# Kernel tuning notes

Measured on AMD Instinct MI355X. Metric: run time of the kernel, lower is better.

The kernel has to match this reference:

```python
import jax, jax.numpy as jnp
import numpy as np

GAMMA = 0.25
GN_EPS = 1e-5


def setup_inputs() -> dict:
    key = jax.random.key(0)
    k1, k2, k3 = jax.random.split(key, 3)
    B, T, C = 16, 2048, 512
    G, V, Dv = 2, 320, 256
    x = jax.random.normal(k1, (B, T, C), dtype=jnp.float32)
    conv_w = jax.random.normal(k2, (G, C // G, C // G), dtype=jnp.float32) * 0.05
    gn_w = jnp.ones((C,), dtype=jnp.float32)
    gn_b = jnp.zeros((C,), dtype=jnp.float32)
    emb = 0.01 * jax.random.normal(k3, (V, G, Dv), dtype=jnp.float32)
    return {"x": x, "conv_w": conv_w, "gn_w": gn_w, "gn_b": gn_b, "emb": emb}


def _vq_forward(x, conv_w, gn_w, gn_b, emb):
    B, T, C = x.shape
    V, G, Dv = emb.shape
    sg = jax.lax.stop_gradient
    # time_first -> BxCxT
    xt = jnp.transpose(x, (0, 2, 1))  # [B,C,T]
    # grouped 1x1 conv (no bias)
    xg = xt.reshape(B, G, C // G, T)
    ze = jnp.einsum('goi,bgit->bgot', conv_w, xg)  # [B,G,C/G,T]
    # Fp32GroupNorm over (C/G, T) per group, biased variance
    zf = ze.astype(jnp.float32)
    mu = jnp.mean(zf, axis=(2, 3), keepdims=True)
    var = jnp.mean(jnp.square(zf - mu), axis=(2, 3), keepdims=True)
    zn = ((zf - mu) * jax.lax.rsqrt(var + GN_EPS)).reshape(B, C, T)
    ze = (zn * gn_w[None, :, None] + gn_b[None, :, None]).astype(ze.dtype)  # [B,C,T]
    # split into groups along feature dim: [B,T,G,Dv]
    ze_ = jnp.transpose(ze.reshape(B, G, Dv, T), (0, 3, 1, 2))
    # squared distances [V,B,T,G] (argmin of ||.||_2 == argmin of ||.||_2^2)
    d2 = (jnp.sum(jnp.square(ze_), axis=-1)[None]
          - 2.0 * jnp.einsum('btgd,vgd->vbtg', ze_, emb)
          + jnp.sum(jnp.square(emb), axis=-1)[:, None, None, :])
    idx = jnp.argmin(d2, axis=0)  # [B,T,G] int
    # gather nearest codewords per group
    zq = emb[idx, jnp.arange(G)[None, None, :]]  # [B,T,G,Dv]
    zq = jnp.transpose(zq.reshape(B, T, C), (0, 2, 1))  # [B,C,T]
    # straight-through
    out = sg(zq) + (ze - sg(ze))  # [B,C,T]
    # code perplexity (no grad)
    probs = jnp.mean(jax.nn.one_hot(sg(idx), V, dtype=jnp.float32), axis=(0, 1))  # [G,V]
    perplexity = jnp.sum(jnp.exp(-jnp.sum(probs * jnp.log(probs + 1e-7), axis=-1)))
    # losses
    zef, zqf = ze.astype(jnp.float32), zq.astype(jnp.float32)
    latent = jnp.mean(jnp.square(zqf - sg(zef)))
    commit = jnp.mean(jnp.square(zef - sg(zqf)))
    loss = latent + GAMMA * commit
    out = jnp.transpose(out, (0, 2, 1))  # back to BxTxC
    return out, loss, perplexity, idx


def reference(x, conv_w, gn_w, gn_b, emb):
    return _vq_forward(x, conv_w, gn_w, gn_b, emb)
```

## Files before the change

kernel.cpp:

```cpp
#include <hip/hip_runtime.h>

#define Bq 16
#define Tq 2048
#define Cq 512
#define Gq 2
#define CGq 256
#define Vq 320
#define Mq 32768
#define LOSS_OFF 16777216
#define PPL_OFF  16777217
#define IDX_OFF  16777218

#define MARGIN 1.75e-4f
#define LIST_CAP 16384
#define LIST2_CAP 1024

#define WS_PCONV 0
#define WS_PLOSS 16384
#define WS_MU    49152
#define WS_RS    49280
#define WS_E2    49408
#define WS_LOSSF 51968
#define WS_CNT   51976
#define WS_CNT2  51980
#define WS_HIST  51984
#define WS_PL2   54544
#define WS_LIST2 70928
#define WS_WSP   131072
#define WS_LISTQ 917504

#define SL(X, r) ((X) * 16 + ((r) ^ ((X) & 7)))

typedef short s16x8 __attribute__((ext_vector_type(8)));
typedef float f32x4v __attribute__((ext_vector_type(4)));

__device__ __forceinline__ void bsplit(float x, unsigned &b1, unsigned &b2) {
    unsigned u = __float_as_uint(x);
    unsigned r1 = (u + 0x7fffu + ((u >> 16) & 1u)) & 0xffff0000u;
    b1 = r1 >> 16;
    float d = x - __uint_as_float(r1);
    unsigned u2 = __float_as_uint(d);
    b2 = (u2 + 0x7fffu + ((u2 >> 16) & 1u)) >> 16;
}

__device__ __forceinline__ void bsplit3(float x, unsigned &h, unsigned &m, unsigned &l) {
    unsigned u = __float_as_uint(x);
    unsigned r1 = (u + 0x7fffu + ((u >> 16) & 1u)) & 0xffff0000u;
    h = r1 >> 16;
    float d1 = x - __uint_as_float(r1);
    unsigned u2 = __float_as_uint(d1);
    unsigned r2 = (u2 + 0x7fffu + ((u2 >> 16) & 1u)) & 0xffff0000u;
    m = r2 >> 16;
    float d2 = d1 - __uint_as_float(r2);
    unsigned u3 = __float_as_uint(d2);
    l = (u3 + 0x7fffu + ((u3 >> 16) & 1u)) >> 16;
}

__global__ __launch_bounds__(256) void k_e2(const float* __restrict__ emb,
                                            float* __restrict__ e2w) {
    int row  = blockIdx.x * 4 + (threadIdx.x >> 6);
    int lane = threadIdx.x & 63;
    float4 v = *(const float4*)(emb + (size_t)row * 256 + lane * 4);
    float s = v.x * v.x + v.y * v.y + v.z * v.z + v.w * v.w;
#pragma unroll
    for (int m = 1; m < 64; m <<= 1) s += __shfl_xor(s, m);
    if (lane == 0) e2w[(row & 1) * Vq + (row >> 1)] = s;
}

__global__ __launch_bounds__(256) void k_wsplit(const float* __restrict__ w,
                                                unsigned char* __restrict__ wsp) {
    int t = blockIdx.x * 256 + threadIdx.x;
    int g = t >> 13, o = (t >> 5) & 255, ihi = t & 31;
    const float* src = w + ((size_t)(g * 256 + o)) * 256 + ihi * 8;
    float xv[8];
    *(float4*)(xv + 0) = *(const float4*)(src);
    *(float4*)(xv + 4) = *(const float4*)(src + 4);
    unsigned ph[4] = {0,0,0,0}, pm[4] = {0,0,0,0}, pl[4] = {0,0,0,0};
#pragma unroll
    for (int e = 0; e < 8; e++) {
        unsigned h, m, l;
        bsplit3(xv[e], h, m, l);
        ph[e >> 1] |= h << ((e & 1) * 16);
        pm[e >> 1] |= m << ((e & 1) * 16);
        pl[e >> 1] |= l << ((e & 1) * 16);
    }
    int kc = ihi >> 2, quad = ihi & 3, ct = o >> 4, lf = o & 15;
    size_t base = (size_t)(g * 3) * 131072 + (size_t)kc * 16384 + ct * 1024 + quad * 256 + lf * 16;
    *(uint4*)(wsp + base + 0 * 131072) = *(uint4*)ph;
    *(uint4*)(wsp + base + 1 * 131072) = *(uint4*)pm;
    *(uint4*)(wsp + base + 2 * 131072) = *(uint4*)pl;
}

__global__ __launch_bounds__(256) void k_esplit(const float* __restrict__ emb,
                                                unsigned char* __restrict__ esp) {
    int t = blockIdx.x * 256 + threadIdx.x;
    int g  = t / 10240;
    int r  = t - g * 10240;
    int kc = r / 1280;
    int r2 = r - kc * 1280;
    int ct = r2 >> 6;
    int r3 = r2 & 63;
    int kq = r3 >> 4, l15 = r3 & 15;
    int v  = ct * 16 + l15;
    int k0 = kc * 32 + kq * 8;
    const float* src = emb + ((size_t)v * 2 + g) * 256 + k0;
    float xv[8];
    *(float4*)(xv + 0) = *(const float4*)(src);
    *(float4*)(xv + 4) = *(const float4*)(src + 4);
    unsigned ph[4] = {0,0,0,0}, pl[4] = {0,0,0,0};
#pragma unroll
    for (int e = 0; e < 8; e++) {
        unsigned h, l;
        bsplit(xv[e], h, l);
        ph[e >> 1] |= h << ((e & 1) * 16);
        pl[e >> 1] |= l << ((e & 1) * 16);
    }
    size_t base = (size_t)g * 327680 + (size_t)kc * 20480
                + (size_t)((ct * 4 + kq) * 16 + l15) * 16;
    *(uint4*)(esp + base) = *(uint4*)ph;
    *(uint4*)(esp + base + 163840) = *(uint4*)pl;
}

__global__ __launch_bounds__(256, 2) void k_convM(const float* __restrict__ x,
    const unsigned char* __restrict__ wsp, float* __restrict__ ze,
    double* __restrict__ pconv)
{
    __shared__ unsigned char lds[73728];
    __shared__ double reds[4], redq[4];
    uint4* Bs = (uint4*)lds;
    uint4* As = (uint4*)(lds + 49152);

    int tid = threadIdx.x, bx = blockIdx.x;
    int mt = bx >> 1, g = bx & 1;
    int m0 = mt * 128;
    int w = tid >> 6, lane = tid & 63;
    int quad = lane >> 4, l15 = lane & 15;
    int arow = tid >> 1, ah = tid & 1;
    int aw = arow >> 5, art = (arow >> 4) & 1, ar = arow & 15;
    const float* xrow = x + (size_t)(m0 + arow) * Cq + g * CGq + ah * 16;
    const unsigned char* wslab = wsp + (size_t)(g * 3) * 131072;

    f32x4v zero4 = {0.f, 0.f, 0.f, 0.f};
    f32x4v acc[2][16];
#pragma unroll
    for (int i = 0; i < 2; i++)
#pragma unroll
        for (int j = 0; j < 16; j++) acc[i][j] = zero4;

    for (int kc = 0; kc < 8; kc++) {
        if (kc) __syncthreads();
#pragma unroll
        for (int j = 0; j < 12; j++) {
            int L = (w * 12 + j) * 1024 + lane * 16;
            int p = L >> 14, r = L & 16383;
            __builtin_amdgcn_global_load_lds(
                (const __attribute__((address_space(1))) void*)(wslab + (size_t)p * 131072 + (size_t)kc * 16384 + r),
                (__attribute__((address_space(3))) void*)(lds + L), 16, 0, 0);
        }
// ... 34 lines not shown
#pragma unroll
            for (int rt = 0; rt < 2; rt++) {
                acc[rt][ct] = __builtin_amdgcn_mfma_f32_16x16x32_bf16(afr[0][rt], b0, acc[rt][ct], 0, 0, 0);
                acc[rt][ct] = __builtin_amdgcn_mfma_f32_16x16x32_bf16(afr[1][rt], b0, acc[rt][ct], 0, 0, 0);
                acc[rt][ct] = __builtin_amdgcn_mfma_f32_16x16x32_bf16(afr[2][rt], b0, acc[rt][ct], 0, 0, 0);
                acc[rt][ct] = __builtin_amdgcn_mfma_f32_16x16x32_bf16(afr[0][rt], b1, acc[rt][ct], 0, 0, 0);
                acc[rt][ct] = __builtin_amdgcn_mfma_f32_16x16x32_bf16(afr[1][rt], b1, acc[rt][ct], 0, 0, 0);
                acc[rt][ct] = __builtin_amdgcn_mfma_f32_16x16x32_bf16(afr[0][rt], b2, acc[rt][ct], 0, 0, 0);
            }
        }
    }

    float s = 0.f, q = 0.f;
    float* zb = ze + (size_t)m0 * Cq + g * CGq;
#pragma unroll
    for (int rt = 0; rt < 2; rt++)
#pragma unroll
    for (int ct = 0; ct < 16; ct++)
#pragma unroll
    for (int j = 0; j < 4; j++) {
        float v = acc[rt][ct][j];
        zb[(size_t)(w * 32 + rt * 16 + quad * 4 + j) * Cq + ct * 16 + l15] = v;
        s += v;
        q = __builtin_fmaf(v, v, q);
    }
    double ds = (double)s, dq = (double)q;
#pragma unroll
    for (int m = 1; m < 64; m <<= 1) { ds += __shfl_xor(ds, m); dq += __shfl_xor(dq, m); }
    if (lane == 0) { reds[w] = ds; redq[w] = dq; }
    __syncthreads();
    if (tid == 0) {
        pconv[bx * 2 + 0] = reds[0] + reds[1] + reds[2] + reds[3];
        pconv[bx * 2 + 1] = redq[0] + redq[1] + redq[2] + redq[3];
    }
}

__global__ __launch_bounds__(256) void k_stats(const double* __restrict__ pconv,
                                               float* __restrict__ muw,
                                               float* __restrict__ rsw) {
    int tid = threadIdx.x;
    int bg = tid >> 3, r = tid & 7;
    int b = bg >> 1, g = bg & 1;
    double s = 0.0, q = 0.0;
    for (int j = r; j < 16; j += 8) {
        int pi = (b * 16 + j) * 2 + g;
        s += pconv[pi * 2 + 0];
        q += pconv[pi * 2 + 1];
    }
#pragma unroll
    for (int m = 1; m < 8; m <<= 1) { s += __shfl_xor(s, m); q += __shfl_xor(q, m); }
    if (r == 0) {
        double mu = s / 524288.0;
        double var = q / 524288.0 - mu * mu;
        double rs = 1.0 / sqrt(var + 1e-5);
        muw[bg] = (float)mu;
        rsw[bg] = (float)rs;
    }
}

__global__ __launch_bounds__(256, 2) void k_distA(const unsigned char* __restrict__ esp,
    const float* __restrict__ gw, const float* __restrict__ gb,
    const float* __restrict__ muw, const float* __restrict__ rsw,
    const float* __restrict__ e2w, float* dout,
    unsigned* __restrict__ cntw, unsigned* __restrict__ cnt2w,
    unsigned long long* __restrict__ listq, unsigned* __restrict__ list2)
{
    __shared__ uint4 Asl[1024];
    __shared__ unsigned char ldsB[40960];
    __shared__ float e2s[Vq];
    uint4* Bsl = (uint4*)ldsB;

    int tid = threadIdx.x, bx = blockIdx.x;
    int mt = bx >> 1, g = bx & 1;
    int m0 = mt * 128;
    int bg = (m0 >> 11) * 2 + g;
    float muf = muw[bg], rsf = rsw[bg];
    int w = tid >> 6, lane = tid & 63;
    int quad = lane >> 4, l15 = lane & 15;

    for (int i = tid; i < Vq; i += 256) e2s[i] = e2w[g * Vq + i];

    int arow = tid >> 1, ah = tid & 1;
    int aw = arow >> 5, art = (arow >> 4) & 1, ar = arow & 15;
    const float* zrow = dout + (size_t)m0 * Cq + g * CGq + (size_t)arow * Cq;
    const unsigned char* eslab = esp + (size_t)g * 327680;

    f32x4v zero4 = {0.f, 0.f, 0.f, 0.f};
    f32x4v acc[2][20];
#pragma unroll
    for (int i = 0; i < 2; i++)
#pragma unroll
        for (int j = 0; j < 20; j++) acc[i][j] = zero4;

    for (int kc8 = 0; kc8 < 8; kc8++) {
        if (kc8) __syncthreads();
        int k0 = kc8 * 32;
#pragma unroll
        for (int j = 0; j < 10; j++) {
            int L = j * 4096 + tid * 16;
            int s = (j >= 5) ? 1 : 0;
            __builtin_amdgcn_global_load_lds(
                (const __attribute__((address_space(1))) void*)(eslab + (size_t)s * 143360 + (size_t)kc8 * 20480 + L),
// ... 37 lines not shown
        for (int ct = 0; ct < 20; ct++) {
            s16x8 b0 = __builtin_bit_cast(s16x8, Bsl[((0*20 + ct)*4 + quad)*16 + l15]);
            s16x8 b1 = __builtin_bit_cast(s16x8, Bsl[((1*20 + ct)*4 + quad)*16 + l15]);
#pragma unroll
            for (int rt = 0; rt < 2; rt++) {
                acc[rt][ct] = __builtin_amdgcn_mfma_f32_16x16x32_bf16(afr[0][rt], b0, acc[rt][ct], 0, 0, 0);
                acc[rt][ct] = __builtin_amdgcn_mfma_f32_16x16x32_bf16(afr[0][rt], b1, acc[rt][ct], 0, 0, 0);
                acc[rt][ct] = __builtin_amdgcn_mfma_f32_16x16x32_bf16(afr[1][rt], b0, acc[rt][ct], 0, 0, 0);
            }
        }
    }

#pragma unroll
    for (int rt = 0; rt < 2; rt++)
#pragma unroll
    for (int j = 0; j < 4; j++) {
        float m1 = 3.402823466e+38f; int i1 = 0;
#pragma unroll
        for (int ct = 0; ct < 20; ct++) {
            float d2a = e2s[ct * 16 + l15] - 2.0f * acc[rt][ct][j];
            if (d2a < m1) { m1 = d2a; i1 = ct * 16 + l15; }
        }
#pragma unroll
        for (int mm = 1; mm < 16; mm <<= 1) {
            float ov = __shfl_xor(m1, mm);
            int   oi = __shfl_xor(i1, mm);
            if (ov < m1 || (ov == m1 && oi < i1)) { m1 = ov; i1 = oi; }
        }
        float thr = m1 + MARGIN;
        unsigned mask = 0;
#pragma unroll
        for (int ct = 0; ct < 20; ct++) {
            float d2a = e2s[ct * 16 + l15] - 2.0f * acc[rt][ct][j];
            if (d2a <= thr) mask |= (1u << ct);
        }
        int cnt = __popc(mask);
#pragma unroll
        for (int mm = 1; mm < 16; mm <<= 1) cnt += __shfl_xor(cnt, mm);
        int mrow = m0 + w * 32 + rt * 16 + quad * 4 + j;
        unsigned q = (unsigned)mrow * 2u + (unsigned)g;
        unsigned flag = 0;
        if (cnt > 1) {
            if ((i1 & 15) == l15) mask &= ~(1u << (i1 >> 4));
            int cl2 = __popc(mask);
            int inc = cl2;
#pragma unroll
            for (int off = 1; off < 16; off <<= 1) {
                int t = __shfl_up(inc, off, 16);
                if (l15 >= off) inc += t;
            }
            int pre = inc - cl2;
            if (cnt <= 5) {
                int pos_ = 0;
                if (l15 == 0) pos_ = (int)atomicAdd(cntw, 1u);
                pos_ = __shfl(pos_, 0, 16);
                if ((unsigned)pos_ < LIST_CAP) {
                    flag = 512u;
                    unsigned long long contrib = 0ull;
                    unsigned mm2 = mask; int k = pre;
                    while (mm2) {
                        int ct2 = __ffs(mm2) - 1; mm2 &= mm2 - 1;
                        contrib |= ((unsigned long long)(unsigned)(ct2 * 16 + l15)) << (20 + 9 * k);
                        k++;
                    }
#pragma unroll
                    for (int mm = 1; mm < 16; mm <<= 1)
                        contrib |= __shfl_xor(contrib, mm);
                    if (l15 == 0)
                        listq[pos_] = (unsigned long long)q
                                    | ((unsigned long long)(unsigned)cnt << 17) | contrib;
                }
            } else {
                if (l15 == 0) {
                    unsigned p2 = atomicAdd(cnt2w, 1u);
                    if (p2 < LIST2_CAP) { list2[p2] = q; flag = 512u; }
                }
            }
        }
        if (l15 == 0) dout[IDX_OFF + q] = __uint_as_float((unsigned)i1 | flag);
    }
}

__global__ __launch_bounds__(256) void k_exS(const float* __restrict__ emb,
    const float* __restrict__ gw, const float* __restrict__ gb,
    const float* __restrict__ muw, const float* __restrict__ rsw,
    const float* __restrict__ e2w, float* dout,
    unsigned* __restrict__ hist, double* __restrict__ ploss)
{
    int tid = threadIdx.x;
    int lane = tid & 63;
    int wid = blockIdx.x * 4 + (tid >> 6);
    int quad = lane >> 2, j = lane & 3;
    int q = wid * 16 + quad;
    int m = q >> 1, g = q & 1;
    int bg = (m >> 11) * 2 + g;
    float muf = muw[bg], rsf = rsw[bg];
    unsigned packed = __float_as_uint(dout[IDX_OFF + q]);
    int flag = (packed >> 9) & 1;
    int v = packed & 511;
    const float* zb  = dout + (size_t)m * Cq + g * CGq;
    const float* gwb = gw + g * CGq;
    const float* gbb = gb + g * CGq;
    const float* eb  = emb + ((size_t)v * Gq + g) * CGq;
    float z2p = 0.f, dp = 0.f;
    for (int kc = 0; kc < 16; kc++) {
        int k0 = kc * 16 + j * 4;
        float4 z  = *(const float4*)(zb + k0);
        float4 gv = *(const float4*)(gwb + k0);
        float4 bv = *(const float4*)(gbb + k0);
        float4 e4 = *(const float4*)(eb + k0);
        float zn0 = __fadd_rn(__fmul_rn(__fmul_rn(__fsub_rn(z.x, muf), rsf), gv.x), bv.x);
        float zn1 = __fadd_rn(__fmul_rn(__fmul_rn(__fsub_rn(z.y, muf), rsf), gv.y), bv.y);
        float zn2 = __fadd_rn(__fmul_rn(__fmul_rn(__fsub_rn(z.z, muf), rsf), gv.z), bv.z);
        float zn3 = __fadd_rn(__fmul_rn(__fmul_rn(__fsub_rn(z.w, muf), rsf), gv.w), bv.w);
        z2p = __builtin_fmaf(zn0, zn0, z2p);
        z2p = __builtin_fmaf(zn1, zn1, z2p);
        z2p = __builtin_fmaf(zn2, zn2, z2p);
        z2p = __builtin_fmaf(zn3, zn3, z2p);
        dp = __builtin_fmaf(zn0, e4.x, dp);
        dp = __builtin_fmaf(zn1, e4.y, dp);
        dp = __builtin_fmaf(zn2, e4.z, dp);
        dp = __builtin_fmaf(zn3, e4.w, dp);
    }
    z2p += __shfl_xor(z2p, 1); z2p += __shfl_xor(z2p, 2);
    dp  += __shfl_xor(dp, 1);  dp  += __shfl_xor(dp, 2);
    float d2 = __fadd_rn(__fsub_rn(z2p, 2.0f * dp), e2w[g * Vq + v]);
    double lp = 0.0;
    if (!flag && j == 0) {
        dout[IDX_OFF + q] = (float)v;
        atomicAdd(&hist[g * Vq + v], 1u);
        lp = (double)d2;
    }
#pragma unroll
    for (int mm = 1; mm < 64; mm <<= 1) lp += __shfl_xor(lp, mm);
    if (lane == 0) ploss[wid] = lp;
}

__global__ __launch_bounds__(256) void k_exF3(const float* __restrict__ emb,
    const float* __restrict__ gw, const float* __restrict__ gb,
    const float* __restrict__ muw, const float* __restrict__ rsw,
    const float* __restrict__ e2w, float* dout,
    unsigned* __restrict__ hist, double* __restrict__ ploss2,
    const unsigned long long* __restrict__ listq, const unsigned* __restrict__ cntw)
{
    int tid = threadIdx.x, lane = tid & 63;
    int gwid = blockIdx.x * 4 + (tid >> 6);
    int cslot = lane >> 2, j = lane & 3;
    unsigned nn = *cntw; if (nn > LIST_CAP) nn = LIST_CAP;
    int n = (int)nn;
    double lacc = 0.0;
    for (int it = gwid; it < n; it += 2048) {
        unsigned long long e = listq[it];
        unsigned q = (unsigned)(e & 0x1FFFFull);
        int cnt = (int)((e >> 17) & 7u);
        int m = (int)(q >> 1), g = (int)(q & 1u);
        int bg = (m >> 11) * 2 + g;
        float muf = muw[bg], rsf = rsw[bg];
        int v = (int)(__float_as_uint(dout[IDX_OFF + q]) & 511u);
        if (cslot >= 1 && cslot < cnt)
            v = (int)((e >> (20 + 9 * (cslot - 1))) & 511ull);
        const float* zb  = dout + (size_t)m * Cq + g * CGq;
        const float* gwb = gw + g * CGq;
        const float* gbb = gb + g * CGq;
        const float* eb  = emb + ((size_t)v * Gq + g) * CGq;
        float z2p = 0.f, dp = 0.f;
        for (int kc = 0; kc < 16; kc++) {
            int k0 = kc * 16 + j * 4;
            float4 z  = *(const float4*)(zb + k0);
            float4 gv = *(const float4*)(gwb + k0);
            float4 bv = *(const float4*)(gbb + k0);
            float4 e4 = *(const float4*)(eb + k0);
            float zn0 = __fadd_rn(__fmul_rn(__fmul_rn(__fsub_rn(z.x, muf), rsf), gv.x), bv.x);
            float zn1 = __fadd_rn(__fmul_rn(__fmul_rn(__fsub_rn(z.y, muf), rsf), gv.y), bv.y);
            float zn2 = __fadd_rn(__fmul_rn(__fmul_rn(__fsub_rn(z.z, muf), rsf), gv.z), bv.z);
            float zn3 = __fadd_rn(__fmul_rn(__fmul_rn(__fsub_rn(z.w, muf), rsf), gv.w), bv.w);
            z2p = __builtin_fmaf(zn0, zn0, z2p);
            z2p = __builtin_fmaf(zn1, zn1, z2p);
            z2p = __builtin_fmaf(zn2, zn2, z2p);
            z2p = __builtin_fmaf(zn3, zn3, z2p);
            dp = __builtin_fmaf(zn0, e4.x, dp);
            dp = __builtin_fmaf(zn1, e4.y, dp);
            dp = __builtin_fmaf(zn2, e4.z, dp);
            dp = __builtin_fmaf(zn3, e4.w, dp);
        }
        z2p += __shfl_xor(z2p, 1); z2p += __shfl_xor(z2p, 2);
        dp  += __shfl_xor(dp, 1);  dp  += __shfl_xor(dp, 2);
        float d2 = __fadd_rn(__fsub_rn(z2p, 2.0f * dp), e2w[g * Vq + v]);
#pragma unroll
        for (int mm = 4; mm < 64; mm <<= 1) {
            float od = __shfl_xor(d2, mm);
            int   ov = __shfl_xor(v, mm);
            if (od < d2 || (od == d2 && ov < v)) { d2 = od; v = ov; }
        }
        if (lane == 0) {
            dout[IDX_OFF + q] = (float)v;
            atomicAdd(&hist[g * Vq + v], 1u);
            lacc += (double)d2;
        }
    }
    if (lane == 0) ploss2[gwid] = lacc;
}

__global__ __launch_bounds__(256) void k_exFslow(const float* __restrict__ emb,
    const float* __restrict__ gw, const float* __restrict__ gb,
    const float* __restrict__ muw, const float* __restrict__ rsw,
    const float* __restrict__ e2w, float* dout,
    unsigned* __restrict__ hist, double* __restrict__ lossf,
    const unsigned* __restrict__ cnt2w, const unsigned* __restrict__ list2)
{
    int tid = threadIdx.x, lane = tid & 63;
    int wid = blockIdx.x * 4 + (tid >> 6);
    unsigned nn = *cnt2w; if (nn > LIST2_CAP) nn = LIST2_CAP;
    int n = (int)nn;
    for (int it = wid; it < n; it += 128) {
        int q = (int)list2[it];
        int m = q >> 1, g = q & 1;
        int bg = (m >> 11) * 2 + g;
        float muf = muw[bg], rsf = rsw[bg];
        const float* zb = dout + (size_t)m * Cq + g * CGq;
        int k0 = lane * 4;
        float4 z  = *(const float4*)(zb + k0);
        float4 gv = *(const float4*)(gw + g * CGq + k0);
        float4 bv = *(const float4*)(gb + g * CGq + k0);
        float zn0 = __fadd_rn(__fmul_rn(__fmul_rn(__fsub_rn(z.x, muf), rsf), gv.x), bv.x);
        float zn1 = __fadd_rn(__fmul_rn(__fmul_rn(__fsub_rn(z.y, muf), rsf), gv.y), bv.y);
        float zn2 = __fadd_rn(__fmul_rn(__fmul_rn(__fsub_rn(z.z, muf), rsf), gv.z), bv.z);
        float zn3 = __fadd_rn(__fmul_rn(__fmul_rn(__fsub_rn(z.w, muf), rsf), gv.w), bv.w);
        float s = 0.f;
        for (int kc = 0; kc < 16; kc++) {
            int src = (lane & 3) + kc * 4;
            float a0 = __shfl(zn0, src), a1 = __shfl(zn1, src);
            float a2 = __shfl(zn2, src), a3 = __shfl(zn3, src);
            s = __builtin_fmaf(a0, a0, s);
            s = __builtin_fmaf(a1, a1, s);
            s = __builtin_fmaf(a2, a2, s);
            s = __builtin_fmaf(a3, a3, s);
        }
        s += __shfl_xor(s, 1); s += __shfl_xor(s, 2);
        float z2 = s;
        float m1 = 3.402823466e+38f; int i1 = 0;
        for (int v = 0; v < Vq; v += 2) {
            const float* e0 = emb + ((size_t)v * Gq + g) * CGq + k0;
            float4 ea = *(const float4*)e0;
            float4 eb4 = *(const float4*)(e0 + Gq * CGq);
            float da = zn0 * ea.x;  da = __builtin_fmaf(zn1, ea.y, da);
            da = __builtin_fmaf(zn2, ea.z, da); da = __builtin_fmaf(zn3, ea.w, da);
            float db = zn0 * eb4.x; db = __builtin_fmaf(zn1, eb4.y, db);
// ... 2 lines not shown
            for (int mm = 1; mm < 64; mm <<= 1) { da += __shfl_xor(da, mm); db += __shfl_xor(db, mm); }
            float d2a = __fadd_rn(__fsub_rn(z2, 2.0f * da), e2w[g * Vq + v]);
            float d2b = __fadd_rn(__fsub_rn(z2, 2.0f * db), e2w[g * Vq + v + 1]);
            if (d2a < m1) { m1 = d2a; i1 = v; }
            if (d2b < m1) { m1 = d2b; i1 = v + 1; }
        }
        if (lane == 0) {
            dout[IDX_OFF + q] = (float)i1;
            atomicAdd(&hist[g * Vq + i1], 1u);
            atomicAdd(lossf, (double)m1);
        }
    }
}

__global__ __launch_bounds__(256) void k_out(const float* __restrict__ emb, float* dout) {
    size_t u = (size_t)blockIdx.x * 256 + threadIdx.x;
    size_t pos = u * 4;
    int m = (int)(pos >> 9);
    int c = (int)(pos & 511);
    int g = c >> 8, d = c & 255;
    int v = (int)dout[IDX_OFF + (size_t)m * Gq + g];
    float4 o = *(const float4*)(emb + ((size_t)(v * 2 + g)) * 256 + d);
    *(float4*)(dout + pos) = o;
}

__global__ __launch_bounds__(256) void k_final(const double* __restrict__ ploss,
                                               const double* __restrict__ ploss2,
                                               const double* __restrict__ lossf,
                                               const unsigned* __restrict__ hist,
                                               float* dout) {
    __shared__ double redl[4], red0[4], red1[4];
    int tid = threadIdx.x;
    double s = 0.0;
    for (int i = tid; i < 4096; i += 256) s += ploss[i];
    for (int i = tid; i < 2048; i += 256) s += ploss2[i];
#pragma unroll
    for (int m = 1; m < 64; m <<= 1) s += __shfl_xor(s, m);
    double e0 = 0.0, e1 = 0.0;
    for (int pid = tid; pid < 640; pid += 256) {
        double p = (double)hist[pid] * (1.0 / 32768.0);
        double t = p * log(p + 1e-7);
        if (pid < 320) e0 += t; else e1 += t;
    }
#pragma unroll
    for (int m = 1; m < 64; m <<= 1) { e0 += __shfl_xor(e0, m); e1 += __shfl_xor(e1, m); }
    int lane = tid & 63, wv_ = tid >> 6;
    if (lane == 0) { redl[wv_] = s; red0[wv_] = e0; red1[wv_] = e1; }
    __syncthreads();
    if (tid == 0) {
        double S  = redl[0] + redl[1] + redl[2] + redl[3] + *lossf;
        double E0 = red0[0] + red0[1] + red0[2] + red0[3];
        double E1 = red1[0] + red1[1] + red1[2] + red1[3];
        dout[LOSS_OFF] = (float)(1.25 * S / 16777216.0);
        dout[PPL_OFF]  = (float)(exp(-E0) + exp(-E1));
    }
}

extern "C" void kernel_launch(void* const* d_in, const int* in_sizes, int n_in,
                              void* d_out, int out_size, void* d_ws, size_t ws_size,
                              hipStream_t stream) {
    const float* x   = (const float*)d_in[0];
    const float* w   = (const float*)d_in[1];
    const float* gw  = (const float*)d_in[2];
    const float* gb  = (const float*)d_in[3];
    const float* emb = (const float*)d_in[4];
    float* dout = (float*)d_out;
    char* ws = (char*)d_ws;
    double* pconv   = (double*)(ws + WS_PCONV);
    double* ploss   = (double*)(ws + WS_PLOSS);
    float* muw      = (float*)(ws + WS_MU);
    float* rsw      = (float*)(ws + WS_RS);
    float* e2w      = (float*)(ws + WS_E2);
    double* lossf   = (double*)(ws + WS_LOSSF);
    unsigned* cntw  = (unsigned*)(ws + WS_CNT);
    unsigned* cnt2w = (unsigned*)(ws + WS_CNT2);
    unsigned* hist  = (unsigned*)(ws + WS_HIST);
    double* ploss2  = (double*)(ws + WS_PL2);
    unsigned* list2 = (unsigned*)(ws + WS_LIST2);
    unsigned char* wsp = (unsigned char*)(ws + WS_WSP);
    unsigned long long* listq = (unsigned long long*)(ws + WS_LISTQ);

    hipMemsetAsync(ws + WS_LOSSF, 0, 2576, stream);
    k_e2<<<160, 256, 0, stream>>>(emb, e2w);
    k_wsplit<<<64, 256, 0, stream>>>(w, wsp);
    k_convM<<<512, 256, 0, stream>>>(x, wsp, dout, pconv);
    k_esplit<<<80, 256, 0, stream>>>(emb, wsp);
    k_stats<<<1, 256, 0, stream>>>(pconv, muw, rsw);
    k_distA<<<512, 256, 0, stream>>>(wsp, gw, gb, muw, rsw, e2w, dout, cntw, cnt2w, listq, list2);
    k_exS<<<1024, 256, 0, stream>>>(emb, gw, gb, muw, rsw, e2w, dout, hist, ploss);
    k_exF3<<<512, 256, 0, stream>>>(emb, gw, gb, muw, rsw, e2w, dout, hist, ploss2, listq, cntw);
    k_exFslow<<<32, 256, 0, stream>>>(emb, gw, gb, muw, rsw, e2w, dout, hist, lossf, cnt2w, list2);
    k_out<<<16384, 256, 0, stream>>>(emb, dout);
    k_final<<<1, 256, 0, stream>>>(ploss, ploss2, lossf, hist, dout);
}
```

Baseline: 186.1 us.

## Fold GroupNorm into codebook and screen distances with single-bf16 raw conv output

Adds a distance pass that works on a bf16 copy of the raw conv output, written by the conv kernel, against a codebook pre-scaled by the GroupNorm weight. The normalization affine is folded into per-code constants (s1, c1) and a per-group scale. This replaces the multi-term bf16-split distance GEMM of the old pass with a single bf16 MFMA pass. It uses a wider screening margin so that near-ties go to the existing exact fallback kernels. The path runs only when the workspace is large enough. It costs an extra 32MB bf16 write in the conv kernel and may flag more rows for the slower exact re-check.

After: 207.6 us. 1.12x slower.

```diff
diff --git a/kernel.cpp b/kernel.cpp
--- a/kernel.cpp
+++ b/kernel.cpp
@@ -11,7 +11,8 @@
 #define PPL_OFF  16777217
 #define IDX_OFF  16777218
 
-#define MARGIN 1.75e-4f
+#define MARGIN  1.75e-4f
+#define MARGIN2 6.0e-3f
 #define LIST_CAP 16384
 #define LIST2_CAP 1024
 
@@ -26,8 +27,12 @@
 #define WS_HIST  51984
 #define WS_PL2   54544
 #define WS_LIST2 70928
+#define WS_S1    75264
+#define WS_C1    77824
 #define WS_WSP   131072
 #define WS_LISTQ 917504
+#define WS_ZESP  1048576
+#define WS_NEED_BIG 34603008ull
 
 #define SL(X, r) ((X) * 16 + ((r) ^ ((X) & 7)))
 
@@ -56,15 +61,38 @@
     l = (u3 + 0x7fffu + ((u3 >> 16) & 1u)) >> 16;
 }
 
-__global__ __launch_bounds__(256) void k_e2(const float* __restrict__ emb,
-                                            float* __restrict__ e2w) {
+__device__ __forceinline__ unsigned short rne16(float x) {
+    unsigned u = __float_as_uint(x);
+    return (unsigned short)((u + 0x7fffu + ((u >> 16) & 1u)) >> 16);
+}
+
+__global__ __launch_bounds__(256) void k_e2x(const float* __restrict__ emb,
+                                             const float* __restrict__ gw,
+                                             const float* __restrict__ gb,
+                                             float* __restrict__ e2w,
+                                             float* __restrict__ s1w,
+                                             float* __restrict__ c1w) {
     int row  = blockIdx.x * 4 + (threadIdx.x >> 6);
     int lane = threadIdx.x & 63;
+    int g = row & 1;
     float4 v = *(const float4*)(emb + (size_t)row * 256 + lane * 4);
     float s = v.x * v.x + v.y * v.y + v.z * v.z + v.w * v.w;
-#pragma unroll
-    for (int m = 1; m < 64; m <<= 1) s += __shfl_xor(s, m);
-    if (lane == 0) e2w[(row & 1) * Vq + (row >> 1)] = s;
+    float4 g4 = *(const float4*)(gw + g * CGq + lane * 4);
+    float4 b4 = *(const float4*)(gb + g * CGq + lane * 4);
+    float c1 = g4.x * v.x + g4.y * v.y + g4.z * v.z + g4.w * v.w;
+    float c2 = b4.x * v.x + b4.y * v.y + b4.z * v.z + b4.w * v.w;
+#pragma unroll
+    for (int m = 1; m < 64; m <<= 1) {
+        s  += __shfl_xor(s, m);
+        c1 += __shfl_xor(c1, m);
+        c2 += __shfl_xor(c2, m);
+    }
+    if (lane == 0) {
+        int idx = g * Vq + (row >> 1);
+        e2w[idx] = s;
+        s1w[idx] = s - 2.0f * c2;
+        c1w[idx] = c1;
+    }
 }
 
 __global__ __launch_bounds__(256) void k_wsplit(const float* __restrict__ w,
@@ -121,9 +149,40 @@
     *(uint4*)(esp + base + 163840) = *(uint4*)pl;
 }
 
+__global__ __launch_bounds__(256) void k_esplitW(const float* __restrict__ emb,
+                                                 const float* __restrict__ gw,
+                                                 unsigned char* __restrict__ esp) {
+    int t = blockIdx.x * 256 + threadIdx.x;
+    int g  = t / 10240;
+    int r  = t - g * 10240;
+    int kc = r / 1280;
+    int r2 = r - kc * 1280;
+    int ct = r2 >> 6;
+    int r3 = r2 & 63;
+    int kq = r3 >> 4, l15 = r3 & 15;
+    int v  = ct * 16 + l15;
+    int k0 = kc * 32 + kq * 8;
+    const float* src = emb + ((size_t)v * 2 + g) * 256 + k0;
+    const float* gws = gw + g * CGq + k0;
+    float xv[8], gv[8];
+    *(float4*)(xv + 0) = *(const float4*)(src);
+    *(float4*)(xv + 4) = *(const float4*)(src + 4);
+    *(float4*)(gv + 0) = *(const float4*)(gws);
+    *(float4*)(gv + 4) = *(const float4*)(gws + 4);
+    unsigned ph[4] = {0,0,0,0};
+#pragma unroll
+    for (int e = 0; e < 8; e++) {
+        unsigned h = rne16(xv[e] * gv[e]);
+        ph[e >> 1] |= (unsigned)h << ((e & 1) * 16);
+    }
+    size_t base = (size_t)g * 163840 + (size_t)kc * 20480
+                + (size_t)((ct * 4 + kq) * 16 + l15) * 16;
+    *(uint4*)(esp + base) = *(uint4*)ph;
+}
+
 __global__ __launch_bounds__(256, 2) void k_convM(const float* __restrict__ x,
     const unsigned char* __restrict__ wsp, float* __restrict__ ze,
-    double* __restrict__ pconv)
+    double* __restrict__ pconv, unsigned short* __restrict__ zesp)
 {
     __shared__ unsigned char lds[73728];
     __shared__ double reds[4], redq[4];
@@ -224,6 +283,27 @@
     if (tid == 0) {
         pconv[bx * 2 + 0] = reds[0] + reds[1] + reds[2] + reds[3];
         pconv[bx * 2 + 1] = redq[0] + redq[1] + redq[2] + redq[3];
+    }
+
+    if (zesp) {
+        unsigned short* t16 = (unsigned short*)lds;
+#pragma unroll
+        for (int rt = 0; rt < 2; rt++)
+#pragma unroll
+        for (int ct = 0; ct < 16; ct++)
+#pragma unroll
+        for (int j = 0; j < 4; j++)
+            t16[w * 8192 + (rt * 16 + quad * 4 + j) * 256 + ct * 16 + l15] =
+                rne16(acc[rt][ct][j]);
+        __syncthreads();
+#pragma unroll
+        for (int i = 0; i < 16; i++) {
+            int p = i * 64 + lane;
+            int row32 = p >> 5, pk = p & 31;
+            uint4 v = *(uint4*)&t16[w * 8192 + row32 * 256 + pk * 8];
+            int grow = m0 + w * 32 + row32;
+            *(uint4*)(zesp + ((size_t)(g * 32768 + grow)) * 256 + pk * 8) = v;
+        }
     }
 }
 
@@ -363,6 +443,132 @@
 #pragma unroll
         for (int ct = 0; ct < 20; ct++) {
             float d2a = e2s[ct * 16 + l15] - 2.0f * acc[rt][ct][j];
+            if (d2a <= thr) mask |= (1u << ct);
+        }
+        int cnt = __popc(mask);
+#pragma unroll
+        for (int mm = 1; mm < 16; mm <<= 1) cnt += __shfl_xor(cnt, mm);
+        int mrow = m0 + w * 32 + rt * 16 + quad * 4 + j;
+        unsigned q = (unsigned)mrow * 2u + (unsigned)g;
+        unsigned flag = 0;
+        if (cnt > 1) {
+            if ((i1 & 15) == l15) mask &= ~(1u << (i1 >> 4));
+            int cl2 = __popc(mask);
+            int inc = cl2;
+#pragma unroll
+            for (int off = 1; off < 16; off <<= 1) {
+                int t = __shfl_up(inc, off, 16);
+                if (l15 >= off) inc += t;
+            }
+            int pre = inc - cl2;
+            if (cnt <= 5) {
+                int pos_ = 0;
+                if (l15 == 0) pos_ = (int)atomicAdd(cntw, 1u);
+                pos_ = __shfl(pos_, 0, 16);
+                if ((unsigned)pos_ < LIST_CAP) {
+                    flag = 512u;
+                    unsigned long long contrib = 0ull;
+                    unsigned mm2 = mask; int k = pre;
+                    while (mm2) {
+                        int ct2 = __ffs(mm2) - 1; mm2 &= mm2 - 1;
+                        contrib |= ((unsigned long long)(unsigned)(ct2 * 16 + l15)) << (20 + 9 * k);
+                        k++;
+                    }
+#pragma unroll
+                    for (int mm = 1; mm < 16; mm <<= 1)
+                        contrib |= __shfl_xor(contrib, mm);
+                    if (l15 == 0)
+                        listq[pos_] = (unsigned long long)q
+                                    | ((unsigned long long)(unsigned)cnt << 17) | contrib;
+                }
+            } else {
+                if (l15 == 0) {
+                    unsigned p2 = atomicAdd(cnt2w, 1u);
+                    if (p2 < LIST2_CAP) { list2[p2] = q; flag = 512u; }
+                }
+            }
+        }
+        if (l15 == 0) dout[IDX_OFF + q] = __uint_as_float((unsigned)i1 | flag);
+    }
+}
+
+__global__ __launch_bounds__(256, 2) void k_distB(const unsigned char* __restrict__ esp,
+    const unsigned short* __restrict__ zesp,
+    const float* __restrict__ muw, const float* __restrict__ rsw,
+    const float* __restrict__ s1w, const float* __restrict__ c1w,
+    float* dout,
+    unsigned* __restrict__ cntw, unsigned* __restrict__ cnt2w,
+    unsigned long long* __restrict__ listq, unsigned* __restrict__ list2)
+{
+    __shared__ unsigned char ldsB[20480];
+    __shared__ float s0s[Vq];
+    uint4* Bsl = (uint4*)ldsB;
+
+    int tid = threadIdx.x, bx = blockIdx.x;
+    int mt = bx >> 1, g = bx & 1;
+    int m0 = mt * 128;
+    int bg = (m0 >> 11) * 2 + g;
+    float muf = muw[bg], rsf = rsw[bg];
+    float beta = 2.0f * rsf;
+    float alpha = beta * muf;
+    int w = tid >> 6, lane = tid & 63;
+    int quad = lane >> 4, l15 = lane & 15;
+
+    for (int i = tid; i < Vq; i += 256)
+        s0s[i] = s1w[g * Vq + i] + alpha * c1w[g * Vq + i];
+
+    const unsigned char* eslab = esp + (size_t)g * 163840;
+    const unsigned short* za0 =
+        zesp + ((size_t)(g * 32768 + m0 + w * 32 + l15)) * 256 + quad * 8;
+
+    f32x4v zero4 = {0.f, 0.f, 0.f, 0.f};
+    f32x4v acc[2][20];
+#pragma unroll
+    for (int i = 0; i < 2; i++)
+#pragma unroll
+        for (int j = 0; j < 20; j++) acc[i][j] = zero4;
+
+    for (int kc8 = 0; kc8 < 8; kc8++) {
+        if (kc8) __syncthreads();
+#pragma unroll
+        for (int j = 0; j < 5; j++) {
+            int L = j * 4096 + tid * 16;
+            __builtin_amdgcn_global_load_lds(
+                (const __attribute__((address_space(1))) void*)(eslab + (size_t)kc8 * 20480 + L),
+                (__attribute__((address_space(3))) void*)(ldsB + L), 16, 0, 0);
+        }
+        s16x8 a0 = *(const s16x8*)(za0 + kc8 * 32);
+        s16x8 a1 = *(const s16x8*)(za0 + 16 * 256 + kc8 * 32);
+        __syncthreads();
+#pragma unroll
+        for (int ct = 0; ct < 20; ct++) {
+            s16x8 b = __builtin_bit_cast(s16x8, Bsl[(ct * 4 + quad) * 16 + l15]);
+            acc[0][ct] = __builtin_amdgcn_mfma_f32_16x16x32_bf16(a0, b, acc[0][ct], 0, 0, 0);
+            acc[1][ct] = __builtin_amdgcn_mfma_f32_16x16x32_bf16(a1, b, acc[1][ct], 0, 0, 0);
+        }
+    }
+
+#pragma unroll
+    for (int rt = 0; rt < 2; rt++)
+#pragma unroll
+    for (int j = 0; j < 4; j++) {
+        float m1 = 3.402823466e+38f; int i1 = 0;
+#pragma unroll
+        for (int ct = 0; ct < 20; ct++) {
+            float d2a = s0s[ct * 16 + l15] - beta * acc[rt][ct][j];
+            if (d2a < m1) { m1 = d2a; i1 = ct * 16 + l15; }
+        }
+#pragma unroll
+        for (int mm = 1; mm < 16; mm <<= 1) {
+            float ov = __shfl_xor(m1, mm);
+            int   oi = __shfl_xor(i1, mm);
+            if (ov < m1 || (ov == m1 && oi < i1)) { m1 = ov; i1 = oi; }
+        }
+        float thr = m1 + MARGIN2;
+        unsigned mask = 0;
+#pragma unroll
+        for (int ct = 0; ct < 20; ct++) {
+            float d2a = s0s[ct * 16 + l15] - beta * acc[rt][ct][j];
             if (d2a <= thr) mask |= (1u << ct);
         }
         int cnt = __popc(mask);
@@ -657,16 +863,24 @@
     unsigned* hist  = (unsigned*)(ws + WS_HIST);
     double* ploss2  = (double*)(ws + WS_PL2);
     unsigned* list2 = (unsigned*)(ws + WS_LIST2);
+    float* s1w      = (float*)(ws + WS_S1);
+    float* c1w      = (float*)(ws + WS_C1);
     unsigned char* wsp = (unsigned char*)(ws + WS_WSP);
     unsigned long long* listq = (unsigned long long*)(ws + WS_LISTQ);
+    unsigned short* zesp = (unsigned short*)(ws + WS_ZESP);
+    bool big = ws_size >= (size_t)WS_NEED_BIG;
 
     hipMemsetAsync(ws + WS_LOSSF, 0, 2576, stream);
-    k_e2<<<160, 256, 0, stream>>>(emb, e2w);
+    k_e2x<<<160, 256, 0, stream>>>(emb, gw, gb, e2w, s1w, c1w);
     k_wsplit<<<64, 256, 0, stream>>>(w, wsp);
-    k_convM<<<512, 256, 0, stream>>>(x, wsp, dout, pconv);
-    k_esplit<<<80, 256, 0, stream>>>(emb, wsp);
+    k_convM<<<512, 256, 0, stream>>>(x, wsp, dout, pconv, big ? zesp : (unsigned short*)nullptr);
+    if (big) k_esplitW<<<80, 256, 0, stream>>>(emb, gw, wsp);
+    else     k_esplit <<<80, 256, 0, stream>>>(emb, wsp);
     k_stats<<<1, 256, 0, stream>>>(pconv, muw, rsw);
-    k_distA<<<512, 256, 0, stream>>>(wsp, gw, gb, muw, rsw, e2w, dout, cntw, cnt2w, listq, list2);
+    if (big)
+        k_distB<<<512, 256, 0, stream>>>(wsp, zesp, muw, rsw, s1w, c1w, dout, cntw, cnt2w, listq, list2);
+    else
+        k_distA<<<512, 256, 0, stream>>>(wsp, gw, gb, muw, rsw, e2w, dout, cntw, cnt2w, listq, list2);
     k_exS<<<1024, 256, 0, stream>>>(emb, gw, gb, muw, rsw, e2w, dout, hist, ploss);
     k_exF3<<<512, 256, 0, stream>>>(emb, gw, gb, muw, rsw, e2w, dout, hist, ploss2, listq, cntw);
     k_exFslow<<<32, 256, 0, stream>>>(emb, gw, gb, muw, rsw, e2w, dout, hist, lossf, cnt2w, list2);
```

## Fuse prep kernels and fold exact-distance epilogue into distance kernel

Applied to the files above, without the earlier changes.

Merges the three small preprocessing kernels (weight split, embedding split, codeword norms) into one launch, moving the embedding split to its own workspace region so it can run before the conv. Folds the per-row exact distance/loss/histogram pass into the tail of the distance kernel using an LDS index buffer, and merges the slow fallback loop into the refinement kernel. This cuts several launches and re-reads of the index array, at the cost of longer, heavier blocks in the distance kernel.

After: 165.2 us. -11.3%, faster.

```diff
diff --git a/kernel.cpp b/kernel.cpp
--- a/kernel.cpp
+++ b/kernel.cpp
@@ -28,6 +28,7 @@
 #define WS_LIST2 70928
 #define WS_WSP   131072
 #define WS_LISTQ 917504
+#define WS_ESP   1048576
 
 #define SL(X, r) ((X) * 16 + ((r) ^ ((X) & 7)))
 
@@ -56,69 +57,69 @@
     l = (u3 + 0x7fffu + ((u3 >> 16) & 1u)) >> 16;
 }
 
-__global__ __launch_bounds__(256) void k_e2(const float* __restrict__ emb,
-                                            float* __restrict__ e2w) {
-    int row  = blockIdx.x * 4 + (threadIdx.x >> 6);
-    int lane = threadIdx.x & 63;
-    float4 v = *(const float4*)(emb + (size_t)row * 256 + lane * 4);
-    float s = v.x * v.x + v.y * v.y + v.z * v.z + v.w * v.w;
-#pragma unroll
-    for (int m = 1; m < 64; m <<= 1) s += __shfl_xor(s, m);
-    if (lane == 0) e2w[(row & 1) * Vq + (row >> 1)] = s;
-}
-
-__global__ __launch_bounds__(256) void k_wsplit(const float* __restrict__ w,
-                                                unsigned char* __restrict__ wsp) {
-    int t = blockIdx.x * 256 + threadIdx.x;
-    int g = t >> 13, o = (t >> 5) & 255, ihi = t & 31;
-    const float* src = w + ((size_t)(g * 256 + o)) * 256 + ihi * 8;
-    float xv[8];
-    *(float4*)(xv + 0) = *(const float4*)(src);
-    *(float4*)(xv + 4) = *(const float4*)(src + 4);
-    unsigned ph[4] = {0,0,0,0}, pm[4] = {0,0,0,0}, pl[4] = {0,0,0,0};
-#pragma unroll
-    for (int e = 0; e < 8; e++) {
-        unsigned h, m, l;
-        bsplit3(xv[e], h, m, l);
-        ph[e >> 1] |= h << ((e & 1) * 16);
-        pm[e >> 1] |= m << ((e & 1) * 16);
-        pl[e >> 1] |= l << ((e & 1) * 16);
-    }
-    int kc = ihi >> 2, quad = ihi & 3, ct = o >> 4, lf = o & 15;
-    size_t base = (size_t)(g * 3) * 131072 + (size_t)kc * 16384 + ct * 1024 + quad * 256 + lf * 16;
-    *(uint4*)(wsp + base + 0 * 131072) = *(uint4*)ph;
-    *(uint4*)(wsp + base + 1 * 131072) = *(uint4*)pm;
-    *(uint4*)(wsp + base + 2 * 131072) = *(uint4*)pl;
-}
-
-__global__ __launch_bounds__(256) void k_esplit(const float* __restrict__ emb,
-                                                unsigned char* __restrict__ esp) {
-    int t = blockIdx.x * 256 + threadIdx.x;
-    int g  = t / 10240;
-    int r  = t - g * 10240;
-    int kc = r / 1280;
-    int r2 = r - kc * 1280;
-    int ct = r2 >> 6;
-    int r3 = r2 & 63;
-    int kq = r3 >> 4, l15 = r3 & 15;
-    int v  = ct * 16 + l15;
-    int k0 = kc * 32 + kq * 8;
-    const float* src = emb + ((size_t)v * 2 + g) * 256 + k0;
-    float xv[8];
-    *(float4*)(xv + 0) = *(const float4*)(src);
-    *(float4*)(xv + 4) = *(const float4*)(src + 4);
-    unsigned ph[4] = {0,0,0,0}, pl[4] = {0,0,0,0};
-#pragma unroll
-    for (int e = 0; e < 8; e++) {
-        unsigned h, l;
-        bsplit(xv[e], h, l);
-        ph[e >> 1] |= h << ((e & 1) * 16);
-        pl[e >> 1] |= l << ((e & 1) * 16);
-    }
-    size_t base = (size_t)g * 327680 + (size_t)kc * 20480
-                + (size_t)((ct * 4 + kq) * 16 + l15) * 16;
-    *(uint4*)(esp + base) = *(uint4*)ph;
-    *(uint4*)(esp + base + 163840) = *(uint4*)pl;
+__global__ __launch_bounds__(256) void k_prep(const float* __restrict__ w,
+                                              const float* __restrict__ emb,
+                                              unsigned char* __restrict__ wsp,
+                                              unsigned char* __restrict__ esp,
+                                              float* __restrict__ e2w) {
+    int bx = blockIdx.x, tid = threadIdx.x;
+    if (bx < 64) {
+        int t = bx * 256 + tid;
+        int g = t >> 13, o = (t >> 5) & 255, ihi = t & 31;
+        const float* src = w + ((size_t)(g * 256 + o)) * 256 + ihi * 8;
+        float xv[8];
+        *(float4*)(xv + 0) = *(const float4*)(src);
+        *(float4*)(xv + 4) = *(const float4*)(src + 4);
+        unsigned ph[4] = {0,0,0,0}, pm[4] = {0,0,0,0}, pl[4] = {0,0,0,0};
+#pragma unroll
+        for (int e = 0; e < 8; e++) {
+            unsigned h, m, l;
+            bsplit3(xv[e], h, m, l);
+            ph[e >> 1] |= h << ((e & 1) * 16);
+            pm[e >> 1] |= m << ((e & 1) * 16);
+            pl[e >> 1] |= l << ((e & 1) * 16);
+        }
+        int kc = ihi >> 2, quad = ihi & 3, ct = o >> 4, lf = o & 15;
+        size_t base = (size_t)(g * 3) * 131072 + (size_t)kc * 16384 + ct * 1024 + quad * 256 + lf * 16;
+        *(uint4*)(wsp + base + 0 * 131072) = *(uint4*)ph;
+        *(uint4*)(wsp + base + 1 * 131072) = *(uint4*)pm;
+        *(uint4*)(wsp + base + 2 * 131072) = *(uint4*)pl;
+    } else if (bx < 224) {
+        int row  = (bx - 64) * 4 + (tid >> 6);
+        int lane = tid & 63;
+        float4 v = *(const float4*)(emb + (size_t)row * 256 + lane * 4);
+        float s = v.x * v.x + v.y * v.y + v.z * v.z + v.w * v.w;
+#pragma unroll
+        for (int m = 1; m < 64; m <<= 1) s += __shfl_xor(s, m);
+        if (lane == 0) e2w[(row & 1) * Vq + (row >> 1)] = s;
+    } else {
+        int t = (bx - 224) * 256 + tid;
+        int g  = t / 10240;
+        int r  = t - g * 10240;
+        int kc = r / 1280;
+        int r2 = r - kc * 1280;
+        int ct = r2 >> 6;
+        int r3 = r2 & 63;
+        int kq = r3 >> 4, l15 = r3 & 15;
+        int v  = ct * 16 + l15;
+        int k0 = kc * 32 + kq * 8;
+        const float* src = emb + ((size_t)v * 2 + g) * 256 + k0;
+        float xv[8];
+        *(float4*)(xv + 0) = *(const float4*)(src);
+        *(float4*)(xv + 4) = *(const float4*)(src + 4);
+        unsigned ph[4] = {0,0,0,0}, pl[4] = {0,0,0,0};
+#pragma unroll
+        for (int e = 0; e < 8; e++) {
+            unsigned h, l;
+            bsplit(xv[e], h, l);
+            ph[e >> 1] |= h << ((e & 1) * 16);
+            pl[e >> 1] |= l << ((e & 1) * 16);
+        }
+        size_t base = (size_t)g * 327680 + (size_t)kc * 20480
+                    + (size_t)((ct * 4 + kq) * 16 + l15) * 16;
+        *(uint4*)(esp + base) = *(uint4*)ph;
+        *(uint4*)(esp + base + 163840) = *(uint4*)pl;
+    }
 }
 
 __global__ __launch_bounds__(256, 2) void k_convM(const float* __restrict__ x,
@@ -253,13 +254,16 @@
 __global__ __launch_bounds__(256, 2) void k_distA(const unsigned char* __restrict__ esp,
     const float* __restrict__ gw, const float* __restrict__ gb,
     const float* __restrict__ muw, const float* __restrict__ rsw,
-    const float* __restrict__ e2w, float* dout,
+    const float* __restrict__ e2w, const float* __restrict__ emb, float* dout,
     unsigned* __restrict__ cntw, unsigned* __restrict__ cnt2w,
-    unsigned long long* __restrict__ listq, unsigned* __restrict__ list2)
+    unsigned long long* __restrict__ listq, unsigned* __restrict__ list2,
+    unsigned* __restrict__ hist, double* __restrict__ ploss)
 {
     __shared__ uint4 Asl[1024];
     __shared__ unsigned char ldsB[40960];
     __shared__ float e2s[Vq];
+    __shared__ unsigned idxl[128];
+    __shared__ double redp[4];
     uint4* Bsl = (uint4*)ldsB;
 
     int tid = threadIdx.x, bx = blockIdx.x;
@@ -408,71 +412,73 @@
                 }
             }
         }
-        if (l15 == 0) dout[IDX_OFF + q] = __uint_as_float((unsigned)i1 | flag);
-    }
-}
-
-__global__ __launch_bounds__(256) void k_exS(const float* __restrict__ emb,
-    const float* __restrict__ gw, const float* __restrict__ gb,
-    const float* __restrict__ muw, const float* __restrict__ rsw,
-    const float* __restrict__ e2w, float* dout,
-    unsigned* __restrict__ hist, double* __restrict__ ploss)
-{
-    int tid = threadIdx.x;
-    int lane = tid & 63;
-    int wid = blockIdx.x * 4 + (tid >> 6);
-    int quad = lane >> 2, j = lane & 3;
-    int q = wid * 16 + quad;
-    int m = q >> 1, g = q & 1;
-    int bg = (m >> 11) * 2 + g;
-    float muf = muw[bg], rsf = rsw[bg];
-    unsigned packed = __float_as_uint(dout[IDX_OFF + q]);
-    int flag = (packed >> 9) & 1;
-    int v = packed & 511;
-    const float* zb  = dout + (size_t)m * Cq + g * CGq;
-    const float* gwb = gw + g * CGq;
-    const float* gbb = gb + g * CGq;
-    const float* eb  = emb + ((size_t)v * Gq + g) * CGq;
-    float z2p = 0.f, dp = 0.f;
-    for (int kc = 0; kc < 16; kc++) {
-        int k0 = kc * 16 + j * 4;
-        float4 z  = *(const float4*)(zb + k0);
-        float4 gv = *(const float4*)(gwb + k0);
-        float4 bv = *(const float4*)(gbb + k0);
-        float4 e4 = *(const float4*)(eb + k0);
-        float zn0 = __fadd_rn(__fmul_rn(__fmul_rn(__fsub_rn(z.x, muf), rsf), gv.x), bv.x);
-        float zn1 = __fadd_rn(__fmul_rn(__fmul_rn(__fsub_rn(z.y, muf), rsf), gv.y), bv.y);
-        float zn2 = __fadd_rn(__fmul_rn(__fmul_rn(__fsub_rn(z.z, muf), rsf), gv.z), bv.z);
-        float zn3 = __fadd_rn(__fmul_rn(__fmul_rn(__fsub_rn(z.w, muf), rsf), gv.w), bv.w);
-        z2p = __builtin_fmaf(zn0, zn0, z2p);
-        z2p = __builtin_fmaf(zn1, zn1, z2p);
-        z2p = __builtin_fmaf(zn2, zn2, z2p);
-        z2p = __builtin_fmaf(zn3, zn3, z2p);
-        dp = __builtin_fmaf(zn0, e4.x, dp);
-        dp = __builtin_fmaf(zn1, e4.y, dp);
-        dp = __builtin_fmaf(zn2, e4.z, dp);
-        dp = __builtin_fmaf(zn3, e4.w, dp);
-    }
-    z2p += __shfl_xor(z2p, 1); z2p += __shfl_xor(z2p, 2);
-    dp  += __shfl_xor(dp, 1);  dp  += __shfl_xor(dp, 2);
-    float d2 = __fadd_rn(__fsub_rn(z2p, 2.0f * dp), e2w[g * Vq + v]);
-    double lp = 0.0;
-    if (!flag && j == 0) {
-        dout[IDX_OFF + q] = (float)v;
-        atomicAdd(&hist[g * Vq + v], 1u);
-        lp = (double)d2;
-    }
-#pragma unroll
-    for (int mm = 1; mm < 64; mm <<= 1) lp += __shfl_xor(lp, mm);
-    if (lane == 0) ploss[wid] = lp;
-}
-
-__global__ __launch_bounds__(256) void k_exF3(const float* __restrict__ emb,
+        if (l15 == 0) {
+            dout[IDX_OFF + q] = __uint_as_float((unsigned)i1 | flag);
+            idxl[mrow - m0] = (unsigned)i1 | flag;
+        }
+    }
+
+    __syncthreads();
+    {
+        int j = tid & 3;
+        int qloc0 = tid >> 2;
+        const float* gwb = gw + g * CGq;
+        const float* gbb = gb + g * CGq;
+        double lacc = 0.0;
+#pragma unroll
+        for (int it = 0; it < 2; it++) {
+            int qloc = qloc0 + it * 64;
+            unsigned packed = idxl[qloc];
+            int flag = (packed >> 9) & 1;
+            int v = (int)(packed & 511u);
+            int mrow = m0 + qloc;
+            const float* zb = dout + (size_t)mrow * Cq + g * CGq;
+            const float* eb = emb + ((size_t)v * Gq + g) * CGq;
+            float z2p = 0.f, dp = 0.f;
+            for (int kc = 0; kc < 16; kc++) {
+                int k0 = kc * 16 + j * 4;
+                float4 z  = *(const float4*)(zb + k0);
+                float4 gv = *(const float4*)(gwb + k0);
+                float4 bv = *(const float4*)(gbb + k0);
+                float4 e4 = *(const float4*)(eb + k0);
+                float zn0 = __fadd_rn(__fmul_rn(__fmul_rn(__fsub_rn(z.x, muf), rsf), gv.x), bv.x);
+                float zn1 = __fadd_rn(__fmul_rn(__fmul_rn(__fsub_rn(z.y, muf), rsf), gv.y), bv.y);
+                float zn2 = __fadd_rn(__fmul_rn(__fmul_rn(__fsub_rn(z.z, muf), rsf), gv.z), bv.z);
+                float zn3 = __fadd_rn(__fmul_rn(__fmul_rn(__fsub_rn(z.w, muf), rsf), gv.w), bv.w);
+                z2p = __builtin_fmaf(zn0, zn0, z2p);
+                z2p = __builtin_fmaf(zn1, zn1, z2p);
+                z2p = __builtin_fmaf(zn2, zn2, z2p);
+                z2p = __builtin_fmaf(zn3, zn3, z2p);
+                dp = __builtin_fmaf(zn0, e4.x, dp);
+                dp = __builtin_fmaf(zn1, e4.y, dp);
+                dp = __builtin_fmaf(zn2, e4.z, dp);
+                dp = __builtin_fmaf(zn3, e4.w, dp);
+            }
+            z2p += __shfl_xor(z2p, 1); z2p += __shfl_xor(z2p, 2);
+            dp  += __shfl_xor(dp, 1);  dp  += __shfl_xor(dp, 2);
+            float d2 = __fadd_rn(__fsub_rn(z2p, 2.0f * dp), e2s[v]);
+            if (!flag && j == 0) {
+                dout[IDX_OFF + (unsigned)(mrow * 2) + (unsigned)g] = (float)v;
+                atomicAdd(&hist[g * Vq + v], 1u);
+                lacc += (double)d2;
+            }
+        }
+#pragma unroll
+        for (int mm = 1; mm < 64; mm <<= 1) lacc += __shfl_xor(lacc, mm);
+        if (lane == 0) redp[w] = lacc;
+        __syncthreads();
+        if (tid == 0) ploss[bx] = redp[0] + redp[1] + redp[2] + redp[3];
+    }
+}
+
+__global__ __launch_bounds__(256) void k_exF(const float* __restrict__ emb,
     const float* __restrict__ gw, const float* __restrict__ gb,
     const float* __restrict__ muw, const float* __restrict__ rsw,
     const float* __restrict__ e2w, float* dout,
     unsigned* __restrict__ hist, double* __restrict__ ploss2,
-    const unsigned long long* __restrict__ listq, const unsigned* __restrict__ cntw)
+    const unsigned long long* __restrict__ listq, const unsigned* __restrict__ cntw,
+    double* __restrict__ lossf,
+    const unsigned* __restrict__ cnt2w, const unsigned* __restrict__ list2)
 {
     int tid = threadIdx.x, lane = tid & 63;
     int gwid = blockIdx.x * 4 + (tid >> 6);
@@ -530,20 +536,10 @@
         }
     }
     if (lane == 0) ploss2[gwid] = lacc;
-}
-
-__global__ __launch_bounds__(256) void k_exFslow(const float* __restrict__ emb,
-    const float* __restrict__ gw, const float* __restrict__ gb,
-    const float* __restrict__ muw, const float* __restrict__ rsw,
-    const float* __restrict__ e2w, float* dout,
-    unsigned* __restrict__ hist, double* __restrict__ lossf,
-    const unsigned* __restrict__ cnt2w, const unsigned* __restrict__ list2)
-{
-    int tid = threadIdx.x, lane = tid & 63;
-    int wid = blockIdx.x * 4 + (tid >> 6);
-    unsigned nn = *cnt2w; if (nn > LIST2_CAP) nn = LIST2_CAP;
-    int n = (int)nn;
-    for (int it = wid; it < n; it += 128) {
+
+    unsigned nn2 = *cnt2w; if (nn2 > LIST2_CAP) nn2 = LIST2_CAP;
+    int n2 = (int)nn2;
+    for (int it = gwid; it < n2; it += 2048) {
         int q = (int)list2[it];
         int m = q >> 1, g = q & 1;
         int bg = (m >> 11) * 2 + g;
@@ -612,7 +608,7 @@
     __shared__ double redl[4], red0[4], red1[4];
     int tid = threadIdx.x;
     double s = 0.0;
-    for (int i = tid; i < 4096; i += 256) s += ploss[i];
+    for (int i = tid; i < 512; i += 256) s += ploss[i];
     for (int i = tid; i < 2048; i += 256) s += ploss2[i];
 #pragma unroll
     for (int m = 1; m < 64; m <<= 1) s += __shfl_xor(s, m);
@@ -659,17 +655,16 @@
     unsigned* list2 = (unsigned*)(ws + WS_LIST2);
     unsigned char* wsp = (unsigned char*)(ws + WS_WSP);
     unsigned long long* listq = (unsigned long long*)(ws + WS_LISTQ);
+    unsigned char* esp = (unsigned char*)(ws + WS_ESP);
 
     hipMemsetAsync(ws + WS_LOSSF, 0, 2576, stream);
-    k_e2<<<160, 256, 0, stream>>>(emb, e2w);
-    k_wsplit<<<64, 256, 0, stream>>>(w, wsp);
+    k_prep<<<304, 256, 0, stream>>>(w, emb, wsp, esp, e2w);
     k_convM<<<512, 256, 0, stream>>>(x, wsp, dout, pconv);
-    k_esplit<<<80, 256, 0, stream>>>(emb, wsp);
     k_stats<<<1, 256, 0, stream>>>(pconv, muw, rsw);
-    k_distA<<<512, 256, 0, stream>>>(wsp, gw, gb, muw, rsw, e2w, dout, cntw, cnt2w, listq, list2);
-    k_exS<<<1024, 256, 0, stream>>>(emb, gw, gb, muw, rsw, e2w, dout, hist, ploss);
-    k_exF3<<<512, 256, 0, stream>>>(emb, gw, gb, muw, rsw, e2w, dout, hist, ploss2, listq, cntw);
-    k_exFslow<<<32, 256, 0, stream>>>(emb, gw, gb, muw, rsw, e2w, dout, hist, lossf, cnt2w, list2);
+    k_distA<<<512, 256, 0, stream>>>(esp, gw, gb, muw, rsw, e2w, emb, dout,
+                                     cntw, cnt2w, listq, list2, hist, ploss);
+    k_exF<<<512, 256, 0, stream>>>(emb, gw, gb, muw, rsw, e2w, dout, hist, ploss2,
+                                   listq, cntw, lossf, cnt2w, list2);
     k_out<<<16384, 256, 0, stream>>>(emb, dout);
     k_final<<<1, 256, 0, stream>>>(ploss, ploss2, lossf, hist, dout);
 }
```
